# Kernel optimization log

Hardware: AMD Instinct MI355X
Metric: run time of the kernel (lower is better)

Reference implementation:

```python
import jax, jax.numpy as jnp
import numpy as np

N = 2048; E = 32768; E2 = 65536; B = 8; P = 20; M = B * P * P * P
NR = 16; SH = 9; FEAT = NR * SH; RE = 64; RH = 128; MC = 32; MH = 16; MODES = 10; CUT = 5.0


def _sh(u):
    # real spherical harmonics l=0,1,2, e3nn 'integral' normalization, on unit vectors u[...,3]
    x, y, z = u[..., 0], u[..., 1], u[..., 2]
    c0 = 0.28209479177387814  # 1/(2 sqrt(pi))
    c1 = 0.4886025119029199   # sqrt(3/(4 pi))
    l0 = jnp.full(x.shape, c0, dtype=u.dtype)
    return jnp.stack([
        l0,
        c1 * y, c1 * z, c1 * x,
        1.0925484305920792 * x * y,
        1.0925484305920792 * y * z,
        0.31539156525252005 * (3.0 * z * z - 1.0),
        1.0925484305920792 * x * z,
        0.5462742152960396 * (x * x - y * y),
    ], axis=-1)


def _gauss(r):
    # soft_one_hot_linspace(basis='gaussian', cutoff=False) * sqrt(RE)
    vals = jnp.linspace(0.0, CUT, RE)
    step = vals[1] - vals[0]
    d = (r[:, None] - vals) / step
    return jnp.exp(-d * d) / 1.12 * np.sqrt(RE)


def _norm_act(x):
    # NormActivation over irreps 16x0e + 16x1 + 16x2 (layout [16 | 16*3 | 16*5])
    s = x[:, :NR]
    v = x[:, NR:NR * 4].reshape(-1, NR, 3)
    t = x[:, NR * 4:].reshape(-1, NR, 5)
    s = s * jax.nn.sigmoid(jnp.abs(s))
    v = v * jax.nn.sigmoid(jnp.linalg.norm(v, axis=-1))[..., None]
    t = t * jax.nn.sigmoid(jnp.linalg.norm(t, axis=-1))[..., None]
    return jnp.concatenate([s, v.reshape(-1, NR * 3), t.reshape(-1, NR * 5)], axis=-1)


def _rmlp(e, m1, m2, m3):
    h = jax.nn.silu(e @ m1)
    h = jax.nn.silu(h @ m2)
    return h @ m3


def _gcn(src, dst, x, sh, emb_e, W, m1, m2, m3, n_dst, Wsc=None):
    # fully-connected tensor-product message passing: gather -> outer(feat, sh) -> GEMM
    # -> radial gate -> scatter-sum; optional self-connection
    xs = x[src]                                                    # [E, Cin]
    msg = (xs[:, :, None] * sh[:, None, :]).reshape(xs.shape[0], -1) @ W
    msg = msg * _rmlp(emb_e, m1, m2, m3)
    out = jax.ops.segment_sum(msg, dst, num_segments=n_dst)
    return out if Wsc is None else out + x @ Wsc


def _spec(x, wr, wi):
    # FNO-style 3D spectral conv on [B,P,P,P,C], low MODES kept in 4 corner blocks
    Px = x.shape[1]
    xf = jnp.fft.rfftn(x, axes=(1, 2, 3))
    w = wr + 1j * wi                                              # [4,C,C,m,m,m]
    m = MODES
    of = jnp.zeros(xf.shape, dtype=xf.dtype)
    corners = [(slice(0, m), slice(0, m)), (slice(-m, None), slice(0, m)),
               (slice(0, m), slice(-m, None)), (slice(-m, None), slice(-m, None))]
    for k, (s1, s2) in enumerate(corners):
        blk = jnp.einsum('bxyzi,ioxyz->bxyzo', xf[:, s1, s2, :m, :], w[k])
        of = of.at[:, s1, s2, :m, :].set(blk)
    return jnp.fft.irfftn(of, s=(Px, Px, Px), axes=(1, 2, 3))


def _forward(pos, cell, emb, g0_W, g0_Wsc, g0_m1, g0_m2, g0_m3,
             g12_W, g12_Wsc, g12_m1, g12_m2, g12_m3,
             a2m_W, a2m_m1, a2m_m2, a2m_m3,
             m2a_W, m2a_m1, m2a_m2, m2a_m3,
             fc0_W, fc0_b, sw_r, sw_i, pw, ff1, ff2, fc1, fc2,
             atomic_numbers, batch, edge_src, edge_dst, atom_src, mesh_dst):
    # atom-atom spherical GCN stack
    ev = pos[edge_src] - pos[edge_dst]
    el = jnp.linalg.norm(ev, axis=-1) + 1e-8
    sh_e = _sh(ev / el[:, None])
    emb_e = _gauss(el)
    x = emb[atomic_numbers]                                        # [N, NR]
    x = _gcn(edge_src, edge_dst, x, sh_e, emb_e, g0_W, g0_m1, g0_m2, g0_m3, N, g0_Wsc)
    for i in range(2):
        x = _norm_act(x)
        x = _gcn(edge_src, edge_dst, x, sh_e, emb_e, g12_W[i], g12_m1[i], g12_m2[i], g12_m3[i], N, g12_Wsc[i])
    # particle mesh positions per cell
    fr = jnp.arange(P) / P
    fg = jnp.stack(jnp.meshgrid(fr, fr, fr, indexing='ij'), axis=-1)   # [P,P,P,3]
    meshpos = jnp.einsum('xyzk,bkl->bxyzl', fg, cell).reshape(-1, 3)   # [M,3]
    # atom -> mesh conv
    ev2 = meshpos[mesh_dst] - pos[atom_src]
    el2 = jnp.linalg.norm(ev2, axis=-1) + 1e-8
    sh2 = _sh(ev2 / el2[:, None])
    emb2 = _gauss(el2)
    mf = _gcn(atom_src, mesh_dst, x, sh2, emb2, a2m_W, a2m_m1, a2m_m2, a2m_m3, M)   # [M, MC]
    mf = mf * jax.nn.sigmoid(jnp.abs(mf))                          # NormActivation on 0e
    mf = mf.reshape(B, P, P, P, MC)
    # PME / FNO mesh conv
    grid = jnp.broadcast_to(fg, (B, P, P, P, 3))
    h = jnp.concatenate([mf, grid], axis=-1) @ fc0_W + fc0_b       # lift to width MH
    for l in range(3):
        h = jax.nn.gelu(_spec(h, sw_r[l], sw_i[l]) + h @ pw[l])
        h = h + jax.nn.gelu(h @ ff1[l]) @ ff2[l]                   # using_ff branch
    h = jax.nn.gelu(h @ fc1) @ fc2                                 # [B,P,P,P,MH]
    mf2 = h.reshape(-1, MH)
    # mesh -> atom conv, per-atom energy, readout
    af = _gcn(mesh_dst, atom_src, mf2, sh2, emb2, m2a_W, m2a_m1, m2a_m2, m2a_m3, N)  # [N,1]
    return jax.ops.segment_sum(af, batch, num_segments=B)          # [B,1]


def setup_inputs():
    key = jax.random.key(0)
    ks = jax.random.split(key, 40)
    r = lambda i, shape, scale: jax.random.normal(ks[i], shape, dtype=jnp.float32) * scale
    inp = {}
    inp['pos'] = jax.random.uniform(ks[0], (N, 3), dtype=jnp.float32) * 10.0
    inp['cell'] = jnp.eye(3, dtype=jnp.float32)[None] * 10.0 + r(1, (B, 3, 3), 0.05)
    inp['atomic_numbers'] = jax.random.randint(ks[2], (N,), 1, 100)
    inp['batch'] = jnp.sort(jax.random.randint(ks[3], (N,), 0, B))
    inp['edge_src'] = jax.random.randint(ks[4], (E,), 0, N)
    inp['edge_dst'] = jax.random.randint(ks[5], (E,), 0, N)
    inp['atom_src'] = jax.random.randint(ks[6], (E2,), 0, N)
    inp['mesh_dst'] = jax.random.randint(ks[7], (E2,), 0, M)
    inp['emb'] = r(8, (100, NR), 1.0)
    inp['g0_W'] = r(9, (NR * SH, FEAT), (NR * SH) ** -0.5)
    inp['g0_Wsc'] = r(10, (NR, FEAT), NR ** -0.5)
    inp['g0_m1'] = r(11, (RE, RH), RE ** -0.5)
    inp['g0_m2'] = r(12, (RH, RH), RH ** -0.5)
    inp['g0_m3'] = r(13, (RH, FEAT), RH ** -0.5)
    inp['g12_W'] = r(14, (2, FEAT * SH, FEAT), (FEAT * SH) ** -0.5)
    inp['g12_Wsc'] = r(15, (2, FEAT, FEAT), FEAT ** -0.5)
    inp['g12_m1'] = r(16, (2, RE, RH), RE ** -0.5)
    inp['g12_m2'] = r(17, (2, RH, RH), RH ** -0.5)
    inp['g12_m3'] = r(18, (2, RH, FEAT), RH ** -0.5)
    inp['a2m_W'] = r(19, (FEAT * SH, MC), (FEAT * SH) ** -0.5)
    inp['a2m_m1'] = r(20, (RE, RH), RE ** -0.5)
    inp['a2m_m2'] = r(21, (RH, RH), RH ** -0.5)
    inp['a2m_m3'] = r(22, (RH, MC), RH ** -0.5)
    inp['m2a_W'] = r(23, (MH * SH, 1), (MH * SH) ** -0.5)
    inp['m2a_m1'] = r(24, (RE, RH), RE ** -0.5)
    inp['m2a_m2'] = r(25, (RH, RH), RH ** -0.5)
    inp['m2a_m3'] = r(26, (RH, 1), RH ** -0.5)
    inp['fc0_W'] = r(27, (MC + 3, MH), (MC + 3) ** -0.5)
    inp['fc0_b'] = jnp.zeros((MH,), dtype=jnp.float32)
    inp['sw_r'] = r(28, (3, 4, MH, MH, MODES, MODES, MODES), 1.0 / MH)
    inp['sw_i'] = r(29, (3, 4, MH, MH, MODES, MODES, MODES), 1.0 / MH)
    inp['pw'] = r(30, (3, MH, MH), MH ** -0.5)
    inp['ff1'] = r(31, (3, MH, 4 * MH), MH ** -0.5)
    inp['ff2'] = r(32, (3, 4 * MH, MH), (4 * MH) ** -0.5)
    inp['fc1'] = r(33, (MH, 128), MH ** -0.5)
    inp['fc2'] = r(34, (128, MH), 128 ** -0.5)
    return inp


def reference(pos, cell, emb, g0_W, g0_Wsc, g0_m1, g0_m2, g0_m3, g12_W, g12_Wsc, g12_m1, g12_m2, g12_m3, a2m_W, a2m_m1, a2m_m2, a2m_m3, m2a_W, m2a_m1, m2a_m2, m2a_m3, fc0_W, fc0_b, sw_r, sw_i, pw, ff1, ff2, fc1, fc2, atomic_numbers, batch, edge_src, edge_dst, atom_src, mesh_dst):
    return _forward(pos, cell, emb, g0_W, g0_Wsc, g0_m1, g0_m2, g0_m3, g12_W, g12_Wsc, g12_m1, g12_m2, g12_m3, a2m_W, a2m_m1, a2m_m2, a2m_m3, m2a_W, m2a_m1, m2a_m2, m2a_m3, fc0_W, fc0_b, sw_r, sw_i, pw, ff1, ff2, fc1, fc2, atomic_numbers, batch, edge_src, edge_dst, atom_src, mesh_dst)
```

## Files before the change

### kernel.cpp

```cpp
#include <hip/hip_runtime.h>
#include <math.h>

#define DEVI __device__ __forceinline__

namespace {

constexpr int N_  = 2048;
constexpr int E_  = 32768;
constexpr int E2_ = 65536;
constexpr int M_  = 64000;
constexpr int NT_ = 4096;
constexpr float TMAX_ = 5.5f;
constexpr float TH_ = TMAX_ / NT_;

DEVI float sigm(float x)  { return 1.0f/(1.0f+expf(-x)); }
DEVI float geluf(float x) {
  float t = tanhf(0.7978845608028654f*(x + 0.044715f*x*x*x));
  return 0.5f*x*(1.0f+t);
}

__global__ void zero_k(float* __restrict__ p, int n){
  int i = blockIdx.x*256 + threadIdx.x;
  if (i < n) p[i] = 0.0f;
}

__global__ void meshpos_k(const float* __restrict__ cell, float* __restrict__ mp){
  int m = blockIdx.x*256 + threadIdx.x;
  if (m >= M_) return;
  int b = m/8000, r = m%8000;
  float fx = (float)(r/400)    * 0.05f;
  float fy = (float)((r/20)%20)* 0.05f;
  float fz = (float)(r%20)     * 0.05f;
  const float* c = cell + b*9;
  mp[(size_t)m*3+0] = fx*c[0] + fy*c[3] + fz*c[6];
  mp[(size_t)m*3+1] = fx*c[1] + fy*c[4] + fz*c[7];
  mp[(size_t)m*3+2] = fx*c[2] + fy*c[5] + fz*c[8];
}

__global__ void edge_geom2_k(const float* __restrict__ Ppos, const int* __restrict__ pi,
                             const float* __restrict__ Qpos, const int* __restrict__ qi,
                             float* __restrict__ sh, float* __restrict__ el_out, int nE){
  int e = blockIdx.x*256 + threadIdx.x;
  if (e >= nE) return;
  int a = pi[e], b = qi[e];
  float ex = Ppos[(size_t)a*3+0] - Qpos[(size_t)b*3+0];
  float ey = Ppos[(size_t)a*3+1] - Qpos[(size_t)b*3+1];
  float ez = Ppos[(size_t)a*3+2] - Qpos[(size_t)b*3+2];
  float el = sqrtf(ex*ex+ey*ey+ez*ez) + 1e-8f;
  el_out[e] = el;
  float x = ex/el, y = ey/el, z = ez/el;
  float* s = sh + (size_t)e*9;
  s[0] = 0.28209479177387814f;
  s[1] = 0.4886025119029199f*y;
  s[2] = 0.4886025119029199f*z;
  s[3] = 0.4886025119029199f*x;
  s[4] = 1.0925484305920792f*x*y;
  s[5] = 1.0925484305920792f*y*z;
  s[6] = 0.31539156525252005f*(3.0f*z*z-1.0f);
  s[7] = 1.0925484305920792f*x*z;
  s[8] = 0.5462742152960396f*(x*x-y*y);
}

__global__ void gather_emb_k(const float* __restrict__ emb, const int* __restrict__ an,
                             float* __restrict__ x16){
  int idx = blockIdx.x*256 + threadIdx.x;
  if (idx >= N_*16) return;
  int n = idx >> 4, f = idx & 15;
  x16[idx] = emb[(size_t)an[n]*16 + f];
}

__global__ void es_k(float* __restrict__ Es){
  int idx = blockIdx.x*256 + threadIdx.x;
  if (idx >= NT_*64) return;
  int r = idx >> 6, k = idx & 63;
  const float step = 5.0f/63.0f;
  float d = (r*TH_ - k*step)/step;
  Es[idx] = expf(-d*d)*(8.0f/1.12f);
}

DEVI float lerp_tab(const float* __restrict__ T, float el, int O, int o){
  float u = el * (1.0f/TH_);
  u = fminf(u, (float)(NT_-1));
  int i = (int)u; if (i > NT_-2) i = NT_-2;
  float f = u - (float)i;
  float t0 = T[(size_t)i*O + o];
  float t1 = T[(size_t)(i+1)*O + o];
  return t0 + f*(t1 - t0);
}

#define BM 64
#define BN 64
#define BK 16

struct BG {
  const float* A[5]; const float* B[5]; float* C[5];
  int K; int Nc[5];
};
template<int ACT>
__global__ __launch_bounds__(256) void bgemm_k(BG args){
  int chain = blockIdx.z;
  const float* A = args.A[chain];
  const float* Bm = args.B[chain];
  float* C = args.C[chain];
  int K = args.K, Nc = args.Nc[chain];
  int row0 = blockIdx.y*BM, col0 = blockIdx.x*BN;
  if (col0 >= Nc) return;
  __shared__ float As[BK][BM+4];
  __shared__ float Bs[BK][BN+4];
  int tid = threadIdx.x;
  int tx = tid & 15, ty = tid >> 4;
  float acc[4][4] = {};
  for (int k0 = 0; k0 < K; k0 += BK) {
    { int kk = tid & 15; int mloc = tid >> 4;
      int gk = k0 + kk;
      for (int p = 0; p < 4; ++p) {
        int m = mloc + p*16; int gm = row0 + m;
        As[kk][m] = A[(size_t)gm*K + gk];
      } }
    { int nn = tid & 63; int kl = tid >> 6;
      for (int p = 0; p < 4; ++p) {
        int kk = kl + p*4; int gk = k0 + kk; int gn = col0 + nn;
        Bs[kk][nn] = (gn < Nc) ? Bm[(size_t)gk*Nc + gn] : 0.0f;
      } }
    __syncthreads();
    #pragma unroll
    for (int kk = 0; kk < BK; ++kk) {
      float a[4], b[4];
      #pragma unroll
      for (int i=0;i<4;++i) a[i] = As[kk][ty*4+i];
      #pragma unroll
      for (int j=0;j<4;++j) b[j] = Bs[kk][tx*4+j];
      #pragma unroll
      for (int i=0;i<4;++i)
        #pragma unroll
        for (int j=0;j<4;++j) acc[i][j] += a[i]*b[j];
    }
    __syncthreads();
  }
  for (int i=0;i<4;++i) {
    int gm = row0 + ty*4+i;
    for (int j=0;j<4;++j) {
      int gn = col0 + tx*4+j; if (gn >= Nc) continue;
      float v = acc[i][j];
      if (ACT==1) v = v*sigm(v);
      C[(size_t)gm*Nc + gn] = v;
    }
  }
}

__global__ __launch_bounds__(256) void gemm_k(const float* __restrict__ A, const float* __restrict__ B,
                      float* __restrict__ C, int Mr, int K, int Nc){
  __shared__ float As[BK][BM+4];
  __shared__ float Bs[BK][BN+4];
  int tid = threadIdx.x;
  int row0 = blockIdx.y*BM, col0 = blockIdx.x*BN;
  int tx = tid & 15, ty = tid >> 4;
  float acc[4][4] = {};
  for (int k0 = 0; k0 < K; k0 += BK) {
    { int kk = tid & 15; int mloc = tid >> 4;
      int gk = k0 + kk;
      for (int p = 0; p < 4; ++p) {
        int m = mloc + p*16; int gm = row0 + m;
        As[kk][m] = (gm < Mr && gk < K) ? A[(size_t)gm*K + gk] : 0.0f;
      } }
    { int nn = tid & 63; int kl = tid >> 6;
      for (int p = 0; p < 4; ++p) {
        int kk = kl + p*4; int gk = k0 + kk; int gn = col0 + nn;
        Bs[kk][nn] = (gk < K && gn < Nc) ? B[(size_t)gk*Nc + gn] : 0.0f;
      } }
    __syncthreads();
    #pragma unroll
    for (int kk = 0; kk < BK; ++kk) {
      float a[4], b[4];
      #pragma unroll
      for (int i=0;i<4;++i) a[i] = As[kk][ty*4+i];
      #pragma unroll
      for (int j=0;j<4;++j) b[j] = Bs[kk][tx*4+j];
      #pragma unroll
      for (int i=0;i<4;++i)
        #pragma unroll
        for (int j=0;j<4;++j) acc[i][j] += a[i]*b[j];
    }
    __syncthreads();
  }
  for (int i=0;i<4;++i) {
    int gm = row0 + ty*4+i; if (gm >= Mr) continue;
    for (int j=0;j<4;++j) {
      int gn = col0 + tx*4+j; if (gn >= Nc) continue;
      C[(size_t)gm*Nc + gn] = acc[i][j];
    }
  }
}

template<int O>
__global__ void wreshape_k(const float* __restrict__ W, float* __restrict__ Wt, int F){
  int idx = blockIdx.x*256 + threadIdx.x;
  int total = F*9*O;
  if (idx >= total) return;
  int o = idx % O; int s = (idx / O) % 9; int f = idx / (9*O);
  Wt[idx] = W[(size_t)(f*9+s)*O + o];
}

template<int O>
__global__ void econtract_k(const float* __restrict__ Y, const int* __restrict__ src,
                            const int* __restrict__ dst, const float* __restrict__ SH,
                            const float* __restrict__ EL, const float* __restrict__ T,
                            float* __restrict__ out, int nE){
  int idx = blockIdx.x*256 + threadIdx.x;
  if (idx >= nE*O) return;
  int e = idx / O, o = idx - e*O;
  const float* sr = SH + (size_t)e*9;
  const float* yr = Y + (size_t)src[e]*(9*O) + o;
  float acc = 0.0f;
  #pragma unroll
  for (int s = 0; s < 9; ++s) acc += sr[s] * yr[s*O];
  float rv = lerp_tab(T, EL[e], O, o);
  atomicAdd(&out[(size_t)dst[e]*O + o], acc * rv);
}

__global__ void normact_k(const float* __restrict__ x, float* __restrict__ y){
  int idx = blockIdx.x*256 + threadIdx.x;
  if (idx >= N_*16) return;
  int n = idx >> 4, r = idx & 15;
  const float* xr = x + (size_t)n*144;
  float* yr = y + (size_t)n*144;
  float s = xr[r];
  yr[r] = s * sigm(fabsf(s));
  float v0 = xr[16+r*3], v1 = xr[16+r*3+1], v2 = xr[16+r*3+2];
  float gv = sigm(sqrtf(v0*v0+v1*v1+v2*v2));
  yr[16+r*3]=v0*gv; yr[16+r*3+1]=v1*gv; yr[16+r*3+2]=v2*gv;
  float t0=xr[64+r*5],t1=xr[64+r*5+1],t2=xr[64+r*5+2],t3=xr[64+r*5+3],t4=xr[64+r*5+4];
  float gt = sigm(sqrtf(t0*t0+t1*t1+t2*t2+t3*t3+t4*t4));
  yr[64+r*5]=t0*gt; yr[64+r*5+1]=t1*gt; yr[64+r*5+2]=t2*gt; yr[64+r*5+3]=t3*gt; yr[64+r*5+4]=t4*gt;
}

__global__ void fc0_k(const float* __restrict__ mf, const float* __restrict__ Wt,
                      const float* __restrict__ bb, float* __restrict__ h){
  int idx = blockIdx.x*256 + threadIdx.x;
  if (idx >= M_*16) return;
  int m = idx >> 4, o = idx & 15;
  int r = m % 8000;
  float fx = (float)(r/400)*0.05f, fy = (float)((r/20)%20)*0.05f, fz = (float)(r%20)*0.05f;
  const float* mfr = mf + (size_t)m*32;
  float acc = bb[o];
  #pragma unroll
  for (int j=0;j<32;++j){
    float v = mfr[j];
    v = v * sigm(fabsf(v));
    acc += v*Wt[j*16+o];
  }
  acc += fx*Wt[32*16+o] + fy*Wt[33*16+o] + fz*Wt[34*16+o];
  h[idx] = acc;
}

__global__ __launch_bounds__(256) void wreorder2_k(const float* __restrict__ wr, const float* __restrict__ wi,
                          float2* __restrict__ W2){
  __shared__ float2 tile[2560];
  int l = blockIdx.y;
  const float* wrl = wr + (size_t)l*1024000;
  const float* wil = wi + (size_t)l*1024000;
  int p = blockIdx.x;
  int ky = p/20, kx = p%20;
  int corner = ((kx>=10)?1:0) + ((ky>=10)?2:0);
  int base2 = corner*256;
  int soff = (kx%10)*100 + (ky%10)*10;
  for (int t = threadIdx.x; t < 2560; t += 256){
    int chunk = t/10, kz = t - chunk*10;
    size_t src = (size_t)(base2 + chunk)*1000 + soff + kz;
    tile[kz*256 + chunk] = make_float2(wrl[src], wil[src]);
  }
  __syncthreads();
  float2* dst = W2 + (size_t)l*1024000 + (size_t)p*2560;
  for (int t = threadIdx.x; t < 2560; t += 256) dst[t] = tile[t];
}

__global__ __launch_bounds__(256) void zyfwd_k(const float* __restrict__ h, float2* __restrict__ cA){
  __shared__ float  pl[20][20][4];
  __shared__ float2 tz[20][10][4];
  __shared__ float2 tw[20];
  int tid = threadIdx.x;
  if (tid < 20){ float a = -6.283185307179586f*tid/20.0f; tw[tid] = make_float2(cosf(a), sinf(a)); }
  int bid = blockIdx.x;
  int b = bid / 80, rem = bid % 80;
  int X = rem >> 2, cg = rem & 3;
  const float* hp = h + (size_t)(b*20+X)*400*16 + cg*4;
  for (int t = tid; t < 400; t += 256) {
    int y = t/20, z = t%20;
    const float4 v = *(const float4*)(hp + (size_t)t*16);
    pl[y][z][0]=v.x; pl[y][z][1]=v.y; pl[y][z][2]=v.z; pl[y][z][3]=v.w;
  }
  __syncthreads();
  for (int t = tid; t < 800; t += 256) {
    int c = t & 3, kz = (t>>2)%10, y = t/40;
    float sr=0.0f, si=0.0f; int j=0;
    for (int z=0; z<20; ++z){
      float v = pl[y][z][c];
      float2 w = tw[j];
      sr += v*w.x; si += v*w.y;
      j += kz; if (j>=20) j-=20;
    }
    tz[y][kz][c] = make_float2(sr,si);
  }
  __syncthreads();
  for (int t = tid; t < 800; t += 256) {
    int c = t & 3, kz = (t>>2)%10, ky = t/40;
    float sr=0.0f, si=0.0f; int j=0;
    for (int y=0; y<20; ++y){
      float2 v = tz[y][kz][c];
      float2 w = tw[j];
      sr += v.x*w.x - v.y*w.y;
      si += v.x*w.y + v.y*w.x;
      j += ky; if (j>=20) j-=20;
    }
    cA[((size_t)((b*20+ky)*10+kz)*20 + X)*16 + cg*4+c] = make_float2(sr,si);
  }
}

__global__ __launch_bounds__(256) void xmix_k(const float2* __restrict__ cA, float2* __restrict__ cB,
                    const float2* __restrict__ W2){
  __shared__ float2 xin[16][20];
  __shared__ float2 Xf[20][16];
  __shared__ float2 Mx[20][16];
  __shared__ float2 twf[20], twi[20];
  int tid = threadIdx.x;
  if (tid < 20){
    float a = -6.283185307179586f*tid/20.0f;
    twf[tid] = make_float2(cosf(a), sinf(a));
    twi[tid] = make_float2(cosf(a), -sinf(a));
  }
  int bid = blockIdx.x;
  int b = bid/200, rem = bid%200;
  int ky = rem/10, kz = rem%10;
  const float2* src = cA + (size_t)((b*20+ky)*10+kz)*320;
  for (int t = tid; t < 320; t += 256){
    int x = t/16, i = t%16;
    xin[i][x] = src[t];
  }
  __syncthreads();
  for (int t = tid; t < 320; t += 256){
    int kx = t/16, i = t%16;
    float sr=0.0f, si=0.0f; int j=0;
    for (int x=0;x<20;++x){
      float2 v = xin[i][x]; float2 w = twf[j];
      sr += v.x*w.x - v.y*w.y; si += v.x*w.y + v.y*w.x;
      j += kx; if (j>=20) j-=20;
    }
    Xf[kx][i] = make_float2(sr,si);
  }
  __syncthreads();
  for (int t = tid; t < 320; t += 256){
    int kx = t/16, o = t%16;
    const float2* wp = W2 + ((size_t)(ky*20+kx)*10 + kz)*256 + o;
    float sr=0.0f, si=0.0f;
    #pragma unroll
    for (int i=0;i<16;++i){
      float2 a = Xf[kx][i];
      float2 w = wp[i*16];
      sr += a.x*w.x - a.y*w.y;
      si += a.x*w.y + a.y*w.x;
    }
    Mx[kx][o] = make_float2(sr,si);
  }
  __syncthreads();
  for (int t = tid; t < 320; t += 256){
    int x = t/16, o = t%16;
    float sr=0.0f, si=0.0f; int j=0;
    for (int kx=0;kx<20;++kx){
      float2 v = Mx[kx][o]; float2 w = twi[j];
      sr += v.x*w.x - v.y*w.y; si += v.x*w.y + v.y*w.x;
      j += x; if (j>=20) j-=20;
    }
    cB[((size_t)((b*20+x)*20+ky)*10+kz)*16 + o] = make_float2(sr,si);
  }
}

__global__ __launch_bounds__(256) void yzinv_k(const float2* __restrict__ cB, float* __restrict__ spec){
  __shared__ float2 ci[20][10][4];
  __shared__ float2 ty[20][10][4];
  __shared__ float2 twi[20];
  int tid = threadIdx.x;
  if (tid < 20){ float a = 6.283185307179586f*tid/20.0f; twi[tid] = make_float2(cosf(a), sinf(a)); }
  int bid = blockIdx.x;
  int b = bid/80, rem = bid%80;
  int X = rem>>2, cg = rem&3;
  const float2* src = cB + (size_t)(b*20+X)*200*16;
  for (int t = tid; t < 800; t += 256){
    int c = t&3, kz = (t>>2)%10, ky = t/40;
    ci[ky][kz][c] = src[(size_t)(ky*10+kz)*16 + cg*4+c];
  }
  __syncthreads();
  for (int t = tid; t < 800; t += 256){
    int c = t&3, kz = (t>>2)%10, y = t/40;
    float sr=0.0f, si=0.0f; int j=0;
    for (int ky=0;ky<20;++ky){
      float2 v = ci[ky][kz][c]; float2 w = twi[j];
      sr += v.x*w.x - v.y*w.y; si += v.x*w.y + v.y*w.x;
      j += y; if (j>=20) j-=20;
    }
    ty[y][kz][c] = make_float2(sr,si);
  }
  __syncthreads();
  float* dst = spec + (size_t)(b*20+X)*400*16 + cg*4;
  for (int t = tid; t < 1600; t += 256){
    int c = t&3, z = (t>>2)%20, y = t/80;
    float acc = ty[y][0][c].x;
    float a2 = 0.0f; int jj = 0;
    for (int kz=1; kz<10; ++kz){
      jj += z; if (jj>=20) jj-=20;
      float2 v = ty[y][kz][c]; float2 w = twi[jj];
      a2 += v.x*w.x - v.y*w.y;
    }
    acc += 2.0f*a2;
    dst[(size_t)(y*20+z)*16 + c] = acc * (1.0f/8000.0f);
  }
}

__global__ __launch_bounds__(256) void ffn3_k(const float* __restrict__ spec, const float* __restrict__ h,
                     const float* __restrict__ pw, const float* __restrict__ ff1,
                     const float* __restrict__ ff2, float* __restrict__ hout){
  __shared__ float spw[256];
  __shared__ float sf1[1024];
  __shared__ float sf2[1024];
  __shared__ float h2s[128][17];
  __shared__ float red[2][128][17];
  int tid = threadIdx.x;
  spw[tid] = pw[tid];
  for (int t = tid; t < 1024; t += 256){ sf1[t]=ff1[t]; sf2[t]=ff2[t]; }
  int rl = tid >> 1, q = tid & 1;
  int m = blockIdx.x*128 + rl;
  const float* hr = h + (size_t)m*16;
  float hl[16];
  #pragma unroll
  for (int i=0;i<16;++i) hl[i] = hr[i];
  __syncthreads();
  const float* sp = spec + (size_t)m*16;
  #pragma unroll
  for (int c=0;c<8;++c){
    int o = q*8+c;
    float acc = sp[o];
    #pragma unroll
    for (int i=0;i<16;++i) acc += hl[i]*spw[i*16+o];
    h2s[rl][o] = geluf(acc);
  }
  __syncthreads();
  float h2l[16];
  #pragma unroll
  for (int i=0;i<16;++i) h2l[i] = h2s[rl][i];
  float part[16] = {};
  for (int kk=0;kk<32;++kk){
    int k = q*32+kk;
    float a0=0.0f, a1=0.0f;
    #pragma unroll
    for (int i=0;i<8;++i){ a0 += h2l[i]*sf1[i*64+k]; a1 += h2l[8+i]*sf1[(8+i)*64+k]; }
    float tk = geluf(a0+a1);
    #pragma unroll
    for (int o=0;o<16;++o) part[o] += tk*sf2[k*16+o];
  }
  #pragma unroll
  for (int o=0;o<16;++o) red[q][rl][o] = part[o];
  __syncthreads();
  #pragma unroll
  for (int c=0;c<8;++c){
    int o = q*8+c;
    hout[(size_t)m*16+o] = h2s[rl][o] + red[0][rl][o] + red[1][rl][o];
  }
}

__global__ __launch_bounds__(256) void fctail3_k(const float* __restrict__ h, const float* __restrict__ fc1,
                        const float* __restrict__ fc2, float* __restrict__ outm){
  __shared__ float s1[2048];
  __shared__ float s2[2048];
  __shared__ float red[2][128][17];
  int tid = threadIdx.x;
  for (int t = tid; t < 2048; t += 256){ s1[t]=fc1[t]; s2[t]=fc2[t]; }
  int rl = tid >> 1, q = tid & 1;
  int m = blockIdx.x*128 + rl;
  const float* hr = h + (size_t)m*16;
  float hl[16];
  #pragma unroll
  for (int i=0;i<16;++i) hl[i] = hr[i];
  __syncthreads();
  float part[16] = {};
  for (int kk=0;kk<64;++kk){
    int k = q*64+kk;
    float a0=0.0f, a1=0.0f;
    #pragma unroll
    for (int i=0;i<8;++i){ a0 += hl[i]*s1[i*128+k]; a1 += hl[8+i]*s1[(8+i)*128+k]; }
    float tk = geluf(a0+a1);
    #pragma unroll
    for (int o=0;o<16;++o) part[o] += tk*s2[k*16+o];
  }
  #pragma unroll
  for (int o=0;o<16;++o) red[q][rl][o] = part[o];
  __syncthreads();
  #pragma unroll
  for (int c=0;c<8;++c){
    int o = q*8+c;
    outm[(size_t)m*16+o] = red[0][rl][o] + red[1][rl][o];
  }
}

__global__ void m2a_k(const float* __restrict__ mf2, const int* __restrict__ mdst,
                      const int* __restrict__ asrc, const float* __restrict__ sh2,
                      const float* __restrict__ Wt, const float* __restrict__ EL,
                      const float* __restrict__ T, float* __restrict__ af){
  int e = blockIdx.x*256 + threadIdx.x;
  if (e >= E2_) return;
  const float* xr = mf2 + (size_t)mdst[e]*16;
  const float* sr = sh2 + (size_t)e*9;
  float sh[9];
  #pragma unroll
  for (int s=0;s<9;++s) sh[s] = sr[s];
  float acc = 0.0f;
  #pragma unroll
  for (int f=0;f<16;++f) {
    float xv = xr[f];
    float dot = 0.0f;
    #pragma unroll
    for (int s=0;s<9;++s) dot += sh[s]*Wt[f*9+s];
    acc += xv*dot;
  }
  float rv = lerp_tab(T, EL[e], 1, 0);
  atomicAdd(&af[asrc[e]], acc*rv);
}

__global__ void bsum_k(const float* __restrict__ af, const int* __restrict__ batch,
                       float* __restrict__ out){
  int n = blockIdx.x*256 + threadIdx.x;
  if (n >= N_) return;
  atomicAdd(&out[batch[n]], af[n]);
}

}

extern "C" void kernel_launch(void* const* d_in, const int* in_sizes, int n_in,
                              void* d_out, int out_size, void* d_ws, size_t ws_size,
                              hipStream_t stream) {
  (void)in_sizes; (void)n_in; (void)out_size; (void)ws_size;
  const float* pos   = (const float*)d_in[0];
  const float* cell  = (const float*)d_in[1];
  const int*   an    = (const int*)d_in[2];
  const int*   batch = (const int*)d_in[3];
  const int*   esrc  = (const int*)d_in[4];
  const int*   edst  = (const int*)d_in[5];
  const int*   asrc  = (const int*)d_in[6];
  const int*   mdst  = (const int*)d_in[7];
  const float* emb   = (const float*)d_in[8];
  const float* g0_W  = (const float*)d_in[9];
  const float* g0_Wsc= (const float*)d_in[10];
  const float* g0_m1 = (const float*)d_in[11];
  const float* g0_m2 = (const float*)d_in[12];
  const float* g0_m3 = (const float*)d_in[13];
  const float* g12_W = (const float*)d_in[14];
  const float* g12_Wsc=(const float*)d_in[15];
  const float* g12_m1= (const float*)d_in[16];
  const float* g12_m2= (const float*)d_in[17];
  const float* g12_m3= (const float*)d_in[18];
  const float* a2m_W = (const float*)d_in[19];
  const float* a2m_m1= (const float*)d_in[20];
  const float* a2m_m2= (const float*)d_in[21];
  const float* a2m_m3= (const float*)d_in[22];
  const float* m2a_W = (const float*)d_in[23];
  const float* m2a_m1= (const float*)d_in[24];
  const float* m2a_m2= (const float*)d_in[25];
  const float* m2a_m3= (const float*)d_in[26];
  const float* fc0_W = (const float*)d_in[27];
  const float* fc0_b = (const float*)d_in[28];
  const float* sw_r  = (const float*)d_in[29];
  const float* sw_i  = (const float*)d_in[30];
  const float* pw    = (const float*)d_in[31];
  const float* ff1   = (const float*)d_in[32];
  const float* ff2   = (const float*)d_in[33];
  const float* fc1   = (const float*)d_in[34];
  const float* fc2   = (const float*)d_in[35];
  float* out = (float*)d_out;

  float* Wp = (float*)d_ws;
  size_t off = 0;
  auto alloc = [&](size_t n){ float* p = Wp + off; off += n; return p; };
  float* meshpos = alloc((size_t)M_*3);
  float* she   = alloc((size_t)E_*9);
  float* ELe   = alloc((size_t)E_);
  float* sh2   = alloc((size_t)E2_*9);
  float* EL2   = alloc((size_t)E2_);
  float* x16   = alloc((size_t)N_*16);
  float* xatom = alloc((size_t)N_*144);
  float* xact  = alloc((size_t)N_*144);
  float* Wt    = alloc((size_t)144*1296);
  float* Yg    = alloc((size_t)N_*1296);
  float* mf    = alloc((size_t)M_*32);
  float* hbuf  = alloc((size_t)M_*16);
  float* htmp  = alloc((size_t)M_*16);
  float2* cA   = (float2*)alloc(1024000);
  float2* cB   = (float2*)alloc(1024000);
  float2* W2   = (float2*)alloc((size_t)3*2048000);
  float* af    = alloc((size_t)N_);
  float* Es    = alloc((size_t)NT_*64);
  float* H1g   = alloc((size_t)5*NT_*128);
  float* H2g   = alloc((size_t)5*NT_*128);
  float* T0    = alloc((size_t)NT_*144);
  float* T1    = alloc((size_t)NT_*144);
  float* T2    = alloc((size_t)NT_*144);
  float* T3    = alloc((size_t)NT_*32);
  float* T4    = alloc((size_t)NT_*1);

  auto g1 = [](int n){ return dim3((unsigned)((n+255)/256)); };
  auto gg = [](int Mr, int Nc){ return dim3((unsigned)((Nc+63)/64), (unsigned)((Mr+63)/64)); };

  zero_k<<<g1(8), 256, 0, stream>>>(out, 8);
  zero_k<<<g1(N_), 256, 0, stream>>>(af, N_);
  zero_k<<<g1(M_*32), 256, 0, stream>>>(mf, M_*32);

  meshpos_k<<<g1(M_), 256, 0, stream>>>(cell, meshpos);
  edge_geom2_k<<<g1(E_), 256, 0, stream>>>(pos, esrc, pos, edst, she, ELe, E_);
  edge_geom2_k<<<g1(E2_), 256, 0, stream>>>(meshpos, mdst, pos, asrc, sh2, EL2, E2_);
  gather_emb_k<<<g1(N_*16), 256, 0, stream>>>(emb, an, x16);

  wreorder2_k<<<dim3(400,3), 256, 0, stream>>>(sw_r, sw_i, W2);

  {
    es_k<<<g1(NT_*64), 256, 0, stream>>>(Es);
    BG l1, l2, l3;
    const float* m1s[5] = {g0_m1, g12_m1, g12_m1+(size_t)64*128, a2m_m1, m2a_m1};
    const float* m2s[5] = {g0_m2, g12_m2, g12_m2+(size_t)128*128, a2m_m2, m2a_m2};
    const float* m3s[5] = {g0_m3, g12_m3, g12_m3+(size_t)128*144, a2m_m3, m2a_m3};
    float* Ts[5] = {T0, T1, T2, T3, T4};
    int NOs[5] = {144, 144, 144, 32, 1};
    for (int c = 0; c < 5; ++c) {
      l1.A[c] = Es;                      l1.B[c] = m1s[c]; l1.C[c] = H1g + (size_t)c*NT_*128; l1.Nc[c] = 128;
      l2.A[c] = H1g + (size_t)c*NT_*128; l2.B[c] = m2s[c]; l2.C[c] = H2g + (size_t)c*NT_*128; l2.Nc[c] = 128;
      l3.A[c] = H2g + (size_t)c*NT_*128; l3.B[c] = m3s[c]; l3.C[c] = Ts[c];                   l3.Nc[c] = NOs[c];
    }
    l1.K = 64; l2.K = 128; l3.K = 128;
    bgemm_k<1><<<dim3(2, NT_/64, 5), 256, 0, stream>>>(l1);
    bgemm_k<1><<<dim3(2, NT_/64, 5), 256, 0, stream>>>(l2);
    bgemm_k<0><<<dim3(3, NT_/64, 5), 256, 0, stream>>>(l3);
  }

  wreshape_k<144><<<g1(16*9*144), 256, 0, stream>>>(g0_W, Wt, 16);
  gemm_k<<<gg(N_,1296), 256, 0, stream>>>(x16, Wt, Yg, N_, 16, 1296);
  gemm_k<<<gg(N_,144), 256, 0, stream>>>(x16, g0_Wsc, xatom, N_, 16, 144);
  econtract_k<144><<<g1(E_*144), 256, 0, stream>>>(Yg, esrc, edst, she, ELe, T0, xatom, E_);

  for (int i = 0; i < 2; ++i) {
    normact_k<<<g1(N_*16), 256, 0, stream>>>(xatom, xact);
    wreshape_k<144><<<g1(144*9*144), 256, 0, stream>>>(g12_W + (size_t)i*1296*144, Wt, 144);
    gemm_k<<<gg(N_,1296), 256, 0, stream>>>(xact, Wt, Yg, N_, 144, 1296);
    gemm_k<<<gg(N_,144), 256, 0, stream>>>(xact, g12_Wsc + (size_t)i*144*144, xatom, N_, 144, 144);
    econtract_k<144><<<g1(E_*144), 256, 0, stream>>>(Yg, esrc, edst, she, ELe, (i==0)?T1:T2, xatom, E_);
  }

  wreshape_k<32><<<g1(144*9*32), 256, 0, stream>>>(a2m_W, Wt, 144);
  gemm_k<<<gg(N_,288), 256, 0, stream>>>(xatom, Wt, Yg, N_, 144, 288);
  econtract_k<32><<<g1(E2_*32), 256, 0, stream>>>(Yg, asrc, mdst, sh2, EL2, T3, mf, E2_);

  fc0_k<<<g1(M_*16), 256, 0, stream>>>(mf, fc0_W, fc0_b, hbuf);
  for (int l = 0; l < 3; ++l) {
    zyfwd_k<<<dim3(640), 256, 0, stream>>>(hbuf, cA);
    xmix_k<<<dim3(1600), 256, 0, stream>>>(cA, cB, W2 + (size_t)l*1024000);
    yzinv_k<<<dim3(640), 256, 0, stream>>>(cB, htmp);
    ffn3_k<<<dim3(500), 256, 0, stream>>>(htmp, hbuf, pw + (size_t)l*256,
                                          ff1 + (size_t)l*1024, ff2 + (size_t)l*1024, hbuf);
  }
  fctail3_k<<<dim3(500), 256, 0, stream>>>(hbuf, fc1, fc2, htmp);

  m2a_k<<<g1(E2_), 256, 0, stream>>>(htmp, mdst, asrc, sh2, m2a_W, EL2, T4, af);
  bsum_k<<<g1(N_), 256, 0, stream>>>(af, batch, out);
}
```

Measured before the change: 595.9 us.

## Widen node GEMM tiles to 64x128, vectorize LDS reads, halve radial table

Replaces the 64x64 node-feature GEMM with a 64x128-tile kernel where each thread computes 4x8 outputs, using float4 global loads for B and float4 shared-memory reads. The batched radial-MLP GEMM also gets float4 shared reads and unrolled loads. The radial lookup-table resolution drops from 4096 to 2048 entries, halving the table-building GEMM work. The coarser table raises interpolation error, and the wider tile wastes work on narrow outputs such as 144 and 288 columns.

```diff
diff --git a/kernel.cpp b/kernel.cpp
--- a/kernel.cpp
+++ b/kernel.cpp
@@ -9,7 +9,7 @@
 constexpr int E_  = 32768;
 constexpr int E2_ = 65536;
 constexpr int M_  = 64000;
-constexpr int NT_ = 4096;
+constexpr int NT_ = 2048;
 constexpr float TMAX_ = 5.5f;
 constexpr float TH_ = TMAX_ / NT_;
 
@@ -88,10 +88,6 @@
   return t0 + f*(t1 - t0);
 }
 
-#define BM 64
-#define BN 64
-#define BK 16
-
 struct BG {
   const float* A[5]; const float* B[5]; float* C[5];
   int K; int Nc[5];
@@ -103,33 +99,34 @@
   const float* Bm = args.B[chain];
   float* C = args.C[chain];
   int K = args.K, Nc = args.Nc[chain];
-  int row0 = blockIdx.y*BM, col0 = blockIdx.x*BN;
+  int row0 = blockIdx.y*64, col0 = blockIdx.x*64;
   if (col0 >= Nc) return;
-  __shared__ float As[BK][BM+4];
-  __shared__ float Bs[BK][BN+4];
+  __shared__ float As[16][72];
+  __shared__ float Bs[16][72];
   int tid = threadIdx.x;
   int tx = tid & 15, ty = tid >> 4;
   float acc[4][4] = {};
-  for (int k0 = 0; k0 < K; k0 += BK) {
+  for (int k0 = 0; k0 < K; k0 += 16) {
     { int kk = tid & 15; int mloc = tid >> 4;
       int gk = k0 + kk;
+      #pragma unroll
       for (int p = 0; p < 4; ++p) {
         int m = mloc + p*16; int gm = row0 + m;
         As[kk][m] = A[(size_t)gm*K + gk];
       } }
     { int nn = tid & 63; int kl = tid >> 6;
+      #pragma unroll
       for (int p = 0; p < 4; ++p) {
         int kk = kl + p*4; int gk = k0 + kk; int gn = col0 + nn;
         Bs[kk][nn] = (gn < Nc) ? Bm[(size_t)gk*Nc + gn] : 0.0f;
       } }
     __syncthreads();
     #pragma unroll
-    for (int kk = 0; kk < BK; ++kk) {
-      float a[4], b[4];
-      #pragma unroll
-      for (int i=0;i<4;++i) a[i] = As[kk][ty*4+i];
-      #pragma unroll
-      for (int j=0;j<4;++j) b[j] = Bs[kk][tx*4+j];
+    for (int kk = 0; kk < 16; ++kk) {
+      float4 a4 = *(const float4*)&As[kk][ty*4];
+      float4 b4 = *(const float4*)&Bs[kk][tx*4];
+      float a[4] = {a4.x,a4.y,a4.z,a4.w};
+      float b[4] = {b4.x,b4.y,b4.z,b4.w};
       #pragma unroll
       for (int i=0;i<4;++i)
         #pragma unroll
@@ -148,45 +145,62 @@
   }
 }
 
-__global__ __launch_bounds__(256) void gemm_k(const float* __restrict__ A, const float* __restrict__ B,
-                      float* __restrict__ C, int Mr, int K, int Nc){
-  __shared__ float As[BK][BM+4];
-  __shared__ float Bs[BK][BN+4];
+__global__ __launch_bounds__(256) void gemm128_k(const float* __restrict__ A, const float* __restrict__ B,
+                        float* __restrict__ C, int Mr, int K, int Nc){
+  __shared__ float As[16][72];
+  __shared__ float Bs[16][136];
   int tid = threadIdx.x;
-  int row0 = blockIdx.y*BM, col0 = blockIdx.x*BN;
+  int row0 = blockIdx.y*64, col0 = blockIdx.x*128;
   int tx = tid & 15, ty = tid >> 4;
-  float acc[4][4] = {};
-  for (int k0 = 0; k0 < K; k0 += BK) {
-    { int kk = tid & 15; int mloc = tid >> 4;
+  float acc[4][8] = {};
+  for (int k0 = 0; k0 < K; k0 += 16) {
+    {
+      int kk = tid & 15, mloc = tid >> 4;
       int gk = k0 + kk;
+      #pragma unroll
       for (int p = 0; p < 4; ++p) {
         int m = mloc + p*16; int gm = row0 + m;
-        As[kk][m] = (gm < Mr && gk < K) ? A[(size_t)gm*K + gk] : 0.0f;
-      } }
-    { int nn = tid & 63; int kl = tid >> 6;
-      for (int p = 0; p < 4; ++p) {
-        int kk = kl + p*4; int gk = k0 + kk; int gn = col0 + nn;
-        Bs[kk][nn] = (gk < K && gn < Nc) ? B[(size_t)gk*Nc + gn] : 0.0f;
-      } }
+        As[kk][m] = (gm < Mr) ? A[(size_t)gm*K + gk] : 0.0f;
+      }
+    }
+    {
+      int nn4 = tid & 31, kk = tid >> 5;
+      #pragma unroll
+      for (int p = 0; p < 2; ++p) {
+        int kkk = kk + p*8;
+        int gk = k0 + kkk;
+        int gn = col0 + nn4*4;
+        float4 v = make_float4(0.f,0.f,0.f,0.f);
+        if (gn + 3 < Nc) {
+          v = *(const float4*)(B + (size_t)gk*Nc + gn);
+        } else if (gn < Nc) {
+          float t0 = B[(size_t)gk*Nc + gn];
+          float t1 = (gn+1<Nc)? B[(size_t)gk*Nc + gn+1] : 0.f;
+          float t2 = (gn+2<Nc)? B[(size_t)gk*Nc + gn+2] : 0.f;
+          v = make_float4(t0,t1,t2,0.f);
+        }
+        *(float4*)&Bs[kkk][nn4*4] = v;
+      }
+    }
     __syncthreads();
     #pragma unroll
-    for (int kk = 0; kk < BK; ++kk) {
-      float a[4], b[4];
-      #pragma unroll
-      for (int i=0;i<4;++i) a[i] = As[kk][ty*4+i];
-      #pragma unroll
-      for (int j=0;j<4;++j) b[j] = Bs[kk][tx*4+j];
+    for (int kk = 0; kk < 16; ++kk) {
+      float4 a4 = *(const float4*)&As[kk][ty*4];
+      float4 b0 = *(const float4*)&Bs[kk][tx*8];
+      float4 b1 = *(const float4*)&Bs[kk][tx*8+4];
+      float av[4] = {a4.x,a4.y,a4.z,a4.w};
+      float bv[8] = {b0.x,b0.y,b0.z,b0.w,b1.x,b1.y,b1.z,b1.w};
       #pragma unroll
       for (int i=0;i<4;++i)
         #pragma unroll
-        for (int j=0;j<4;++j) acc[i][j] += a[i]*b[j];
+        for (int j=0;j<8;++j) acc[i][j] += av[i]*bv[j];
     }
     __syncthreads();
   }
-  for (int i=0;i<4;++i) {
-    int gm = row0 + ty*4+i; if (gm >= Mr) continue;
-    for (int j=0;j<4;++j) {
-      int gn = col0 + tx*4+j; if (gn >= Nc) continue;
+  for (int i=0;i<4;++i){
+    int gm = row0 + ty*4 + i; if (gm >= Mr) continue;
+    for (int j=0;j<8;++j){
+      int gn = col0 + tx*8 + j; if (gn >= Nc) continue;
       C[(size_t)gm*Nc + gn] = acc[i][j];
     }
   }
@@ -605,7 +619,7 @@
   float* T4    = alloc((size_t)NT_*1);
 
   auto g1 = [](int n){ return dim3((unsigned)((n+255)/256)); };
-  auto gg = [](int Mr, int Nc){ return dim3((unsigned)((Nc+63)/64), (unsigned)((Mr+63)/64)); };
+  auto gg2 = [](int Mr, int Nc){ return dim3((unsigned)((Nc+127)/128), (unsigned)((Mr+63)/64)); };
 
   zero_k<<<g1(8), 256, 0, stream>>>(out, 8);
   zero_k<<<g1(N_), 256, 0, stream>>>(af, N_);
@@ -638,20 +652,20 @@
   }
 
   wreshape_k<144><<<g1(16*9*144), 256, 0, stream>>>(g0_W, Wt, 16);
-  gemm_k<<<gg(N_,1296), 256, 0, stream>>>(x16, Wt, Yg, N_, 16, 1296);
-  gemm_k<<<gg(N_,144), 256, 0, stream>>>(x16, g0_Wsc, xatom, N_, 16, 144);
+  gemm128_k<<<gg2(N_,1296), 256, 0, stream>>>(x16, Wt, Yg, N_, 16, 1296);
+  gemm128_k<<<gg2(N_,144), 256, 0, stream>>>(x16, g0_Wsc, xatom, N_, 16, 144);
   econtract_k<144><<<g1(E_*144), 256, 0, stream>>>(Yg, esrc, edst, she, ELe, T0, xatom, E_);
 
   for (int i = 0; i < 2; ++i) {
     normact_k<<<g1(N_*16), 256, 0, stream>>>(xatom, xact);
     wreshape_k<144><<<g1(144*9*144), 256, 0, stream>>>(g12_W + (size_t)i*1296*144, Wt, 144);
-    gemm_k<<<gg(N_,1296), 256, 0, stream>>>(xact, Wt, Yg, N_, 144, 1296);
-    gemm_k<<<gg(N_,144), 256, 0, stream>>>(xact, g12_Wsc + (size_t)i*144*144, xatom, N_, 144, 144);
+    gemm128_k<<<gg2(N_,1296), 256, 0, stream>>>(xact, Wt, Yg, N_, 144, 1296);
+    gemm128_k<<<gg2(N_,144), 256, 0, stream>>>(xact, g12_Wsc + (size_t)i*144*144, xatom, N_, 144, 144);
     econtract_k<144><<<g1(E_*144), 256, 0, stream>>>(Yg, esrc, edst, she, ELe, (i==0)?T1:T2, xatom, E_);
   }
 
   wreshape_k<32><<<g1(144*9*32), 256, 0, stream>>>(a2m_W, Wt, 144);
-  gemm_k<<<gg(N_,288), 256, 0, stream>>>(xatom, Wt, Yg, N_, 144, 288);
+  gemm128_k<<<gg2(N_,288), 256, 0, stream>>>(xatom, Wt, Yg, N_, 144, 288);
   econtract_k<32><<<g1(E2_*32), 256, 0, stream>>>(Yg, asrc, mdst, sh2, EL2, T3, mf, E2_);
 
   fc0_k<<<g1(M_*16), 256, 0, stream>>>(mf, fc0_W, fc0_b, hbuf);
```

Result: slower. 610.4 us (+2.4%).
